# Optimization experiments

Measured on AMD Instinct MI355X. Metric: run time of the kernel, lower is better.

## Reference

```python
import jax, jax.numpy as jnp
import numpy as np
from jax import lax

B_, L_ = 4, 512
D_MODEL, N_LAYER = 384, 4
D_INNER, N_STATE, DT_RANK, D_CONV = 768, 16, 24, 4
VOCAB, FEAT = 1544, 1536


def setup_inputs() -> dict:
    key = jax.random.key(0)
    ks = iter(jax.random.split(key, 32))
    nrm = lambda shape, s=0.02: jax.random.normal(next(ks), shape, jnp.float32) * s
    input_ids = jax.random.normal(next(ks), (B_, L_, VOCAB), jnp.float32)
    return dict(
        input_ids=input_ids,
        fc_W=nrm((D_MODEL, VOCAB)), fc_b=jnp.zeros((D_MODEL,), jnp.float32),
        in_proj_W=nrm((N_LAYER, 2 * D_INNER, D_MODEL)),
        conv_W=nrm((N_LAYER, D_INNER, 1, D_CONV), 0.2),
        conv_b=jnp.zeros((N_LAYER, D_INNER), jnp.float32),
        x_proj_W=nrm((N_LAYER, DT_RANK + 2 * N_STATE, D_INNER)),
        dt_proj_W=nrm((N_LAYER, D_INNER, DT_RANK)),
        dt_proj_b=jnp.zeros((N_LAYER, D_INNER), jnp.float32),
        A_log=jnp.tile(jnp.log(jnp.arange(1, N_STATE + 1, dtype=jnp.float32)), (N_LAYER, D_INNER, 1)),
        D=jnp.ones((N_LAYER, D_INNER), jnp.float32),
        out_proj_W=nrm((N_LAYER, D_MODEL, D_INNER)),
        norm_W=jnp.ones((N_LAYER, D_MODEL), jnp.float32),
        normf_W=jnp.ones((D_MODEL,), jnp.float32),
        head_W=nrm((FEAT, D_MODEL)),
    )


def _rmsnorm(x, w, eps=1e-5):
    return x * lax.rsqrt(jnp.mean(x * x, axis=-1, keepdims=True) + eps) * w


def _selective_scan(u, delta, A, B, C, D):
    # u, delta: (b, l, d); A: (d, n); B, C: (b, l, n); D: (d,)
    dA = jnp.exp(jnp.einsum('bld,dn->bldn', delta, A))          # (b, l, d, n)
    dBu = jnp.einsum('bld,bln->bldn', delta * u, B)             # (b, l, d, n)
    b, l, d = u.shape
    n = A.shape[1]

    def step(h, inp):
        dA_t, dBu_t, c_t = inp                                   # (b,d,n),(b,d,n),(b,n)
        h = dA_t * h + dBu_t
        y = jnp.einsum('bdn,bn->bd', h, c_t)
        return h, y

    h0 = jnp.zeros((b, d, n), u.dtype)
    _, ys = lax.scan(step, h0, (dA.transpose(1, 0, 2, 3), dBu.transpose(1, 0, 2, 3), C.transpose(1, 0, 2)))
    return ys.transpose(1, 0, 2) + u * D                         # (b, l, d)


def _mamba(input_ids, fc_W, fc_b, in_proj_W, conv_W, conv_b, x_proj_W,
           dt_proj_W, dt_proj_b, A_log, D, out_proj_W, norm_W, normf_W, head_W):
    x = input_ids @ fc_W.T + fc_b                                # (b, l, d_model)
    for i in range(N_LAYER):
        h = _rmsnorm(x, norm_W[i])
        xz = h @ in_proj_W[i].T                                  # (b, l, 2*d_inner)
        xc, res = jnp.split(xz, 2, axis=-1)
        xc = xc.transpose(0, 2, 1)                               # (b, d_inner, l)
        xc = lax.conv_general_dilated(
            xc, conv_W[i], window_strides=(1,), padding=[(D_CONV - 1, 0)],
            feature_group_count=D_INNER, dimension_numbers=('NCH', 'OIH', 'NCH'))
        xc = xc + conv_b[i][None, :, None]
        u = jax.nn.silu(xc.transpose(0, 2, 1))                   # (b, l, d_inner)
        x_dbl = u @ x_proj_W[i].T
        delta, Bm, Cm = jnp.split(x_dbl, [DT_RANK, DT_RANK + N_STATE], axis=-1)
        delta = jax.nn.softplus(delta @ dt_proj_W[i].T + dt_proj_b[i])
        A = -jnp.exp(A_log[i])
        y = _selective_scan(u, delta, A, Bm, Cm, D[i])
        y = y * jax.nn.silu(res)
        x = y @ out_proj_W[i].T + x                              # residual
    x = _rmsnorm(x, normf_W)
    return x @ head_W.T                                          # (b, l, feat)


def reference(input_ids, fc_W, fc_b, in_proj_W, conv_W, conv_b, x_proj_W,
              dt_proj_W, dt_proj_b, A_log, D, out_proj_W, norm_W, normf_W, head_W):
    return _mamba(input_ids, fc_W, fc_b, in_proj_W, conv_W, conv_b, x_proj_W,
                  dt_proj_W, dt_proj_b, A_log, D, out_proj_W, norm_W, normf_W, head_W)
```

## Files before the change

### kernel.cpp

```cpp
#include <hip/hip_runtime.h>
#include <math.h>

#define B_ 4
#define L_ 512
#define MROWS 2048
#define D_MODEL 384
#define N_LAYER 4
#define D_INNER 768
#define N_STATE 16
#define DT_RANK 24
#define D_CONV 4
#define VOCAB 1544
#define FEAT 1536
#define XPROJ_N 56
#define NCH 16
#define SCH 32
#define DG 2

typedef __attribute__((ext_vector_type(8))) short short8;
typedef __attribute__((ext_vector_type(4))) float floatx4;

__device__ __forceinline__ float softplus_f(float x) { return x > 20.f ? x : log1pf(expf(x)); }
__device__ __forceinline__ float silu_f(float x) { return x / (1.f + __expf(-x)); }

__device__ __forceinline__ unsigned pack2bf(float x, float y) {
    unsigned ux = __float_as_uint(x); ux = (ux + 0x7FFFu + ((ux >> 16) & 1u)) >> 16;
    unsigned uy = __float_as_uint(y); uy = (uy + 0x7FFFu + ((uy >> 16) & 1u)) >> 16;
    return ux | (uy << 16);
}

template <int CTRL>
__device__ __forceinline__ float dpp_radd(float x) {
    int r = __builtin_amdgcn_update_dpp(0, __float_as_int(x), CTRL, 0xf, 0xf, true);
    return x + __int_as_float(r);
}

__device__ __forceinline__ void wave_lds_fence() {
    asm volatile("s_waitcnt lgkmcnt(0)" ::: "memory");
    __builtin_amdgcn_wave_barrier();
}

__device__ __forceinline__ short8 ld8h_guard(const short* __restrict__ p, int k, int ke) {
    if (k + 7 < ke) return *(const short8*)(p + k);
    short8 r = {0, 0, 0, 0, 0, 0, 0, 0};
#pragma unroll
    for (int j = 0; j < 8; ++j)
        if (k + j < ke) r[j] = p[k + j];
    return r;
}

struct CastDesc {
    const float* src[6];
    short*       dst[6];
    unsigned     cum[6];
};

__global__ __launch_bounds__(256) void cast_w_k(CastDesc cd, unsigned total4,
                                                float4* __restrict__ zb, unsigned z4)
{
    unsigned i = blockIdx.x * 256 + threadIdx.x;
    if (i < total4) {
        int s = 0;
#pragma unroll
        for (int j = 0; j < 5; ++j)
            if (i >= cd.cum[j] && s == j) s = j + 1;
        unsigned off = i - (s ? cd.cum[s - 1] : 0u);
        float4 v = ((const float4*)cd.src[s])[off];
        uint2 pk;
        pk.x = pack2bf(v.x, v.y);
        pk.y = pack2bf(v.z, v.w);
        ((uint2*)cd.dst[s])[off] = pk;
    } else {
        unsigned zi = i - total4;
        if (zi < z4) zb[zi] = make_float4(0.f, 0.f, 0.f, 0.f);
    }
}

__global__ __launch_bounds__(256) void rmsnorm_cast_k(
    const float* __restrict__ x, const float* __restrict__ nw,
    unsigned* __restrict__ outp)
{
    const int idx = blockIdx.x * 256 + threadIdx.x;
    const int row = idx >> 3, q = idx & 7;
    const float* xr = x + (size_t)row * D_MODEL + q * 48;
    float4 v[12];
    float s = 0.f;
#pragma unroll
    for (int i = 0; i < 12; ++i) {
        v[i] = *(const float4*)(xr + i * 4);
        s += v[i].x * v[i].x + v[i].y * v[i].y + v[i].z * v[i].z + v[i].w * v[i].w;
    }
    s += __shfl_xor(s, 1, 64);
    s += __shfl_xor(s, 2, 64);
    s += __shfl_xor(s, 4, 64);
    const float sc = rsqrtf(s / (float)D_MODEL + 1e-5f);
    unsigned* op = outp + ((size_t)row * D_MODEL + q * 48) / 2;
#pragma unroll
    for (int i = 0; i < 12; ++i) {
        float4 wv = *(const float4*)(nw + q * 48 + i * 4);
        op[i * 2]     = pack2bf(v[i].x * (sc * wv.x), v[i].y * (sc * wv.y));
        op[i * 2 + 1] = pack2bf(v[i].z * (sc * wv.z), v[i].w * (sc * wv.w));
    }
}

#define ASTR 40

template <int EPI, bool ATOMIC, bool NG, bool ABF>
__global__ __launch_bounds__(256) void mfma_gemm(
    const float* __restrict__ A, const short* __restrict__ Abf,
    const short* __restrict__ Wb,
    const float* __restrict__ bias,
    float* __restrict__ C, int M, int N, int K, int lda, int ldc, int KC)
{
    __shared__ short As[2][64 * ASTR];
    __shared__ short Ws[2][64 * ASTR];

    const int t  = threadIdx.x;
    const int m0 = blockIdx.y * 64;
    const int n0 = blockIdx.x * 64;
    const int ks = blockIdx.z * KC;
    const int ke = min(K, ks + KC);

    const int srow = t >> 2;
    const int sseg = (t & 3) * 8;

    short8 ra8, rw8;

    auto prefetch = [&](int k0) {
        ra8 = ld8h_guard(Abf + (size_t)(m0 + srow) * lda, k0 + sseg, ke);
        if (!NG || (n0 + srow) < N) {
            rw8 = ld8h_guard(Wb + (size_t)(n0 + srow) * (size_t)K, k0 + sseg, ke);
        } else {
            rw8 = (short8){0, 0, 0, 0, 0, 0, 0, 0};
        }
    };

    auto stage = [&](int p) {
        *(short8*)&As[p][srow * ASTR + sseg] = ra8;
        *(short8*)&Ws[p][srow * ASTR + sseg] = rw8;
    };

    prefetch(ks);
    stage(0);
    if (ks + 32 < ke) prefetch(ks + 32);
    __syncthreads();

    floatx4 acc[2][2];
#pragma unroll
    for (int i = 0; i < 2; ++i)
#pragma unroll
        for (int j = 0; j < 2; ++j) acc[i][j] = (floatx4){0.f, 0.f, 0.f, 0.f};

    const int w    = t >> 6;
    const int lane = t & 63;
    const int quad = lane >> 4;
    const int lm   = lane & 15;
    const int aoff = ((w >> 1) * 32 + lm) * ASTR + quad * 8;
    const int boff = ((w & 1) * 32 + lm) * ASTR + quad * 8;

    int p = 0;
    for (int k0 = ks; k0 < ke; k0 += 32) {
        const bool more = (k0 + 32 < ke);
        if (more) {
            stage(p ^ 1);
            if (k0 + 64 < ke) prefetch(k0 + 64);
        }
        short8 a0 = *(const short8*)&As[p][aoff];
        short8 a1 = *(const short8*)&As[p][aoff + 16 * ASTR];
        short8 b0 = *(const short8*)&Ws[p][boff];
        short8 b1 = *(const short8*)&Ws[p][boff + 16 * ASTR];
        acc[0][0] = __builtin_amdgcn_mfma_f32_16x16x32_bf16(a0, b0, acc[0][0], 0, 0, 0);
        acc[0][1] = __builtin_amdgcn_mfma_f32_16x16x32_bf16(a0, b1, acc[0][1], 0, 0, 0);
        acc[1][0] = __builtin_amdgcn_mfma_f32_16x16x32_bf16(a1, b0, acc[1][0], 0, 0, 0);
        acc[1][1] = __builtin_amdgcn_mfma_f32_16x16x32_bf16(a1, b1, acc[1][1], 0, 0, 0);
        if (more) {
            __syncthreads();
            p ^= 1;
        }
    }

    const int rbase = m0 + (w >> 1) * 32 + quad * 4;
    const int cbase = n0 + (w & 1) * 32 + lm;
#pragma unroll
    for (int mt = 0; mt < 2; ++mt)
#pragma unroll
        for (int nt = 0; nt < 2; ++nt) {
            const int gc = cbase + nt * 16;
            if (NG && gc >= N) continue;
#pragma unroll
            for (int r = 0; r < 4; ++r) {
                const size_t gr = rbase + mt * 16 + r;
                float v = acc[mt][nt][r];
                if (ATOMIC) {
                    if (EPI == 1 && blockIdx.z == 0) v += bias[gc];
                    atomicAdd(&C[gr * ldc + gc], v);
                } else {
                    if (EPI == 1) v += bias[gc];
                    if (EPI == 2) v = softplus_f(v + bias[gc]);
                    C[gr * ldc + gc] = v;
                }
            }
        }
}

__global__ __launch_bounds__(256) void conv_silu_k(
    const float* __restrict__ xz, const float* __restrict__ w,
    const float* __restrict__ cb, float* __restrict__ u, short* __restrict__ ubf)
{
    int idx = blockIdx.x * 256 + threadIdx.x;
    if (idx >= MROWS * (D_INNER / 4)) return;
    int dq = idx % (D_INNER / 4);
    int m  = idx / (D_INNER / 4);
    int d0 = dq * 4;
    int b = m / L_, l = m % L_;
    float4 wq[4];
#pragma unroll
    for (int j = 0; j < 4; ++j) wq[j] = *(const float4*)(w + (d0 + j) * D_CONV);
    float acc[4];
#pragma unroll
    for (int j = 0; j < 4; ++j) acc[j] = cb[d0 + j];
#pragma unroll
    for (int tt = 0; tt < 4; ++tt) {
        int ll = l - 3 + tt;
        if (ll >= 0) {
            float4 xv = *(const float4*)(xz + (size_t)(b * L_ + ll) * (2 * D_INNER) + d0);
            acc[0] = fmaf(xv.x, ((const float*)&wq[0])[tt], acc[0]);
            acc[1] = fmaf(xv.y, ((const float*)&wq[1])[tt], acc[1]);
            acc[2] = fmaf(xv.z, ((const float*)&wq[2])[tt], acc[2]);
            acc[3] = fmaf(xv.w, ((const float*)&wq[3])[tt], acc[3]);
        }
    }
    float4 o = make_float4(silu_f(acc[0]), silu_f(acc[1]), silu_f(acc[2]), silu_f(acc[3]));
    *(float4*)(u + (size_t)m * D_INNER + d0) = o;
    uint2 pk;
    pk.x = pack2bf(o.x, o.y);
    pk.y = pack2bf(o.z, o.w);
    *(uint2*)(ubf + (size_t)m * D_INNER + d0) = pk;
}

__global__ __launch_bounds__(512, 4) void scan_fused_k(
    const float* __restrict__ xdbl, const float* __restrict__ u,
    const float* __restrict__ xz,
    const float* __restrict__ dtW, const float* __restrict__ dtb,
    const float* __restrict__ A_log, const float* __restrict__ Dp,
    short* __restrict__ ybf)
{
    __shared__ __align__(16) float2 sdu[NCH][SCH][DG];
    __shared__ __align__(16) float  sy[NCH][SCH][DG];
    __shared__ __align__(16) float2 sPH[NCH][DG][16];

    const int t  = threadIdx.x;
    const int w  = t >> 6;
    const int l  = t & 63;
    const int ch = l >> 5;
    const int c  = w * 2 + ch;
    const int dl = (l >> 4) & 1;
    const int n  = l & 15;
    const int bx  = blockIdx.x;
    const int dgi = (bx & 7) * (D_INNER / DG / 8) + (bx >> 3);
    const int d0 = dgi * DG;
    const int d  = d0 + dl;
    const int b  = blockIdx.y;

    const int tc = t >> 5, tj = t & 31;
    const size_t trow = (size_t)b * L_ + t;

    float2 rv  = *(const float2*)(xz + trow * (2 * D_INNER) + D_INNER + d0);
    float2 uv2 = *(const float2*)(u + trow * D_INNER + d0);
    float2 Dv  = *(const float2*)(Dp + d0);

    {
        const float* wd = dtW + (size_t)d0 * DT_RANK;
        const float* xr = xdbl + trow * XPROJ_N;
        float acc0 = dtb[d0];
        float acc1 = dtb[d0 + 1];
#pragma unroll
        for (int q = 0; q < 6; ++q) {
            float4 xv = *(const float4*)(xr + q * 4);
            float4 w0 = *(const float4*)(wd + q * 4);
            float4 w1 = *(const float4*)(wd + DT_RANK + q * 4);
            acc0 = fmaf(xv.x, w0.x, acc0); acc0 = fmaf(xv.y, w0.y, acc0);
            acc0 = fmaf(xv.z, w0.z, acc0); acc0 = fmaf(xv.w, w0.w, acc0);
            acc1 = fmaf(xv.x, w1.x, acc1); acc1 = fmaf(xv.y, w1.y, acc1);
            acc1 = fmaf(xv.z, w1.z, acc1); acc1 = fmaf(xv.w, w1.w, acc1);
        }
        float4 pk = make_float4(softplus_f(acc0), uv2.x, softplus_f(acc1), uv2.y);
        *(float4*)&sdu[tc][tj][0] = pk;
    }
    wave_lds_fence();

    const float Av = -expf(A_log[d * N_STATE + n]);
    const float* xbn = xdbl + ((size_t)b * L_ + c * SCH) * XPROJ_N + DT_RANK + n;

    float eA[SCH], cc[SCH];
    {
        float h = 0.f, sdv = 0.f;
        float rB[8];
#pragma unroll
        for (int q = 0; q < 8; ++q) rB[q] = xbn[q * XPROJ_N];
#pragma unroll
        for (int g = 0; g < SCH / 8; ++g) {
            float nB[8];
            if (g + 1 < SCH / 8) {
#pragma unroll
                for (int q = 0; q < 8; ++q) nB[q] = xbn[(g * 8 + 8 + q) * XPROJ_N];
            }
#pragma unroll
            for (int q = 0; q < 8; ++q) {
                const int j = g * 8 + q;
                float2 du = *(const float2*)&sdu[c][j][dl];
                float e  = __expf(du.x * Av);
                float tt = du.x * du.y * rB[q];
                eA[j] = e;
                cc[j] = tt;
                h = fmaf(e, h, tt);
                sdv += du.x;
            }
#pragma unroll
            for (int q = 0; q < 8; ++q) rB[q] = nB[q];
        }
        float2 ph;
        ph.x = __expf(sdv * Av);
        ph.y = h;
        *(float2*)&sPH[c][dl][n] = ph;
    }

    float rC[8];
#pragma unroll
    for (int q = 0; q < 8; ++q) rC[q] = xbn[q * XPROJ_N + N_STATE];
    __syncthreads();

    float hs = 0.f;
#pragma unroll
    for (int s = 0; s < NCH - 1; ++s) {
        float2 ph = *(const float2*)&sPH[s][dl][n];
        const bool m = s < c;
        hs = fmaf(m ? ph.x : 1.f, hs, m ? ph.y : 0.f);
    }

    {
        float h = hs;
#pragma unroll
        for (int g = 0; g < SCH / 8; ++g) {
            float nC[8];
            if (g + 1 < SCH / 8) {
#pragma unroll
                for (int q = 0; q < 8; ++q)
                    nC[q] = xbn[(g * 8 + 8 + q) * XPROJ_N + N_STATE];
            }
#pragma unroll
            for (int q = 0; q < 8; ++q) {
                const int j = g * 8 + q;
                h = fmaf(eA[j], h, cc[j]);
                float p = h * rC[q];
                p = dpp_radd<0x128>(p);
                p = dpp_radd<0x124>(p);
                p = dpp_radd<0x122>(p);
                p = dpp_radd<0x121>(p);
                if (n == 0) sy[c][j][dl] = p;
            }
#pragma unroll
            for (int q = 0; q < 8; ++q) rC[q] = nC[q];
        }
    }
    wave_lds_fence();

    {
        float2 yv = *(const float2*)&sy[tc][tj][0];
        float y0 = fmaf(uv2.x, Dv.x, yv.x);
        float y1 = fmaf(uv2.y, Dv.y, yv.y);
        float o0 = y0 * silu_f(rv.x);
        float o1 = y1 * silu_f(rv.y);
        *(unsigned*)(ybf + trow * D_INNER + d0) = pack2bf(o0, o1);
    }
}

extern "C" void kernel_launch(void* const* d_in, const int* in_sizes, int n_in,
                              void* d_out, int out_size, void* d_ws, size_t ws_size,
                              hipStream_t stream)
{
    const float* input_ids = (const float*)d_in[0];
    const float* fc_W      = (const float*)d_in[1];
    const float* fc_b      = (const float*)d_in[2];
    const float* in_proj_W = (const float*)d_in[3];
    const float* conv_W    = (const float*)d_in[4];
    const float* conv_b    = (const float*)d_in[5];
    const float* x_proj_W  = (const float*)d_in[6];
    const float* dt_proj_W = (const float*)d_in[7];
    const float* dt_proj_b = (const float*)d_in[8];
    const float* A_log     = (const float*)d_in[9];
    const float* Dp        = (const float*)d_in[10];
    const float* out_proj_W= (const float*)d_in[11];
    const float* norm_W    = (const float*)d_in[12];
    const float* normf_W   = (const float*)d_in[13];
    const float* head_W    = (const float*)d_in[14];
    float* out = (float*)d_out;

    float* ws       = (float*)d_ws;
    float* x_ws     = ws;
    float* xdbl_ws  = x_ws    + (size_t)MROWS * D_MODEL;
    float* xz_ws    = xdbl_ws + (size_t)N_LAYER * MROWS * XPROJ_N;
    float* u_ws     = xz_ws   + (size_t)MROWS * 2 * D_INNER;
    short* bf       = (short*)(u_ws + (size_t)MROWS * D_INNER);
    short* wbf_fc   = bf;
    short* wbf_in   = wbf_fc  + (size_t)D_MODEL * VOCAB;
    short* wbf_x    = wbf_in  + (size_t)N_LAYER * 2 * D_INNER * D_MODEL;
    short* wbf_out  = wbf_x   + (size_t)N_LAYER * XPROJ_N * D_INNER;
    short* wbf_head = wbf_out + (size_t)N_LAYER * D_MODEL * D_INNER;
    short* ids_bf   = wbf_head+ (size_t)FEAT * D_MODEL;
    short* ubf_ws   = ids_bf  + (size_t)MROWS * VOCAB;
    short* ybf_ws   = ubf_ws  + (size_t)MROWS * D_INNER;
    short* xnorm_bf = ybf_ws  + (size_t)MROWS * D_INNER;

    const dim3 blk(256);
    const dim3 blk512(512);

    CastDesc cd;
    cd.src[0] = fc_W;       cd.dst[0] = wbf_fc;
    cd.src[1] = in_proj_W;  cd.dst[1] = wbf_in;
    cd.src[2] = x_proj_W;   cd.dst[2] = wbf_x;
    cd.src[3] = out_proj_W; cd.dst[3] = wbf_out;
    cd.src[4] = head_W;     cd.dst[4] = wbf_head;
    cd.src[5] = input_ids;  cd.dst[5] = ids_bf;
    unsigned c0 = (unsigned)(D_MODEL * VOCAB / 4);
    unsigned c1 = c0 + (unsigned)(N_LAYER * 2 * D_INNER * D_MODEL / 4);
    unsigned c2 = c1 + (unsigned)(N_LAYER * XPROJ_N * D_INNER / 4);
    unsigned c3 = c2 + (unsigned)(N_LAYER * D_MODEL * D_INNER / 4);
    unsigned c4 = c3 + (unsigned)(FEAT * D_MODEL / 4);
    unsigned c5 = c4 + (unsigned)(MROWS * VOCAB / 4);
    cd.cum[0] = c0; cd.cum[1] = c1; cd.cum[2] = c2;
    cd.cum[3] = c3; cd.cum[4] = c4; cd.cum[5] = c5;
    const unsigned zero4 = (unsigned)((MROWS * D_MODEL + N_LAYER * MROWS * XPROJ_N) / 4);
    cast_w_k<<<(c5 + zero4 + 255) / 256, blk, 0, stream>>>(cd, c5, (float4*)x_ws, zero4);

    mfma_gemm<1, true, false, true><<<dim3(D_MODEL / 64, MROWS / 64, 7), blk, 0, stream>>>(
        nullptr, ids_bf, wbf_fc, fc_b, x_ws,
        MROWS, D_MODEL, VOCAB, VOCAB, D_MODEL, 256);

    for (int i = 0; i < N_LAYER; ++i) {
        float* xdbl_i = xdbl_ws + (size_t)i * MROWS * XPROJ_N;

        rmsnorm_cast_k<<<MROWS * 8 / 256, blk, 0, stream>>>(
            x_ws, norm_W + i * D_MODEL, (unsigned*)xnorm_bf);

        mfma_gemm<0, false, false, true><<<dim3(2 * D_INNER / 64, MROWS / 64, 1), blk, 0, stream>>>(
            nullptr, xnorm_bf, wbf_in + (size_t)i * 2 * D_INNER * D_MODEL,
            nullptr, xz_ws,
            MROWS, 2 * D_INNER, D_MODEL, D_MODEL, 2 * D_INNER, D_MODEL);

        conv_silu_k<<<(MROWS * (D_INNER / 4) + 255) / 256, blk, 0, stream>>>(
            xz_ws, conv_W + (size_t)i * D_INNER * D_CONV, conv_b + i * D_INNER,
            u_ws, ubf_ws);

        mfma_gemm<0, true, true, true><<<dim3(1, MROWS / 64, 6), blk, 0, stream>>>(
            nullptr, ubf_ws, wbf_x + (size_t)i * XPROJ_N * D_INNER,
            nullptr, xdbl_i,
            MROWS, XPROJ_N, D_INNER, D_INNER, XPROJ_N, 128);

        scan_fused_k<<<dim3(D_INNER / DG, B_), blk512, 0, stream>>>(
            xdbl_i, u_ws, xz_ws,
            dt_proj_W + (size_t)i * D_INNER * DT_RANK, dt_proj_b + i * D_INNER,
            A_log + (size_t)i * D_INNER * N_STATE, Dp + i * D_INNER, ybf_ws);

        mfma_gemm<0, true, false, true><<<dim3(D_MODEL / 64, MROWS / 64, 2), blk, 0, stream>>>(
            nullptr, ybf_ws, wbf_out + (size_t)i * D_MODEL * D_INNER,
            nullptr, x_ws,
            MROWS, D_MODEL, D_INNER, D_INNER, D_MODEL, 384);
    }

    rmsnorm_cast_k<<<MROWS * 8 / 256, blk, 0, stream>>>(
        x_ws, normf_W, (unsigned*)xnorm_bf);
    mfma_gemm<0, false, false, true><<<dim3(FEAT / 64, MROWS / 64, 1), blk, 0, stream>>>(
        nullptr, xnorm_bf, wbf_head, nullptr, out,
        MROWS, FEAT, D_MODEL, D_MODEL, FEAT, D_MODEL);
}
```

Baseline: 437.8 us.

## Fuse depthwise conv+SiLU into the x_proj MFMA GEMM prologue

Replaces the separate conv_silu kernel and the x_proj GEMM with one kernel. It loads a 67-row xz slab into shared memory, computes the causal depthwise conv and SiLU, writes u in fp32, and feeds bf16 u straight into the MFMA tiles, with split-K atomics into xdbl. This drops one launch per layer plus the bf16 u buffer's write and read. In exchange the K loop is serialized with extra syncs, and each block redoes a small overlap of conv work for its halo rows. The unused fp32-A template parameter is also removed from the GEMM.

```diff
diff --git a/kernel.cpp b/kernel.cpp
--- a/kernel.cpp
+++ b/kernel.cpp
@@ -105,9 +105,9 @@
 
 #define ASTR 40
 
-template <int EPI, bool ATOMIC, bool NG, bool ABF>
+template <int EPI, bool ATOMIC, bool NG>
 __global__ __launch_bounds__(256) void mfma_gemm(
-    const float* __restrict__ A, const short* __restrict__ Abf,
+    const short* __restrict__ Abf,
     const short* __restrict__ Wb,
     const float* __restrict__ bias,
     float* __restrict__ C, int M, int N, int K, int lda, int ldc, int KC)
@@ -203,39 +203,127 @@
         }
 }
 
-__global__ __launch_bounds__(256) void conv_silu_k(
-    const float* __restrict__ xz, const float* __restrict__ w,
-    const float* __restrict__ cb, float* __restrict__ u, short* __restrict__ ubf)
+__global__ __launch_bounds__(256) void xproj_conv_k(
+    const float* __restrict__ xz, const short* __restrict__ Wb,
+    const float* __restrict__ cw, const float* __restrict__ cbp,
+    float* __restrict__ u, float* __restrict__ xdbl)
 {
-    int idx = blockIdx.x * 256 + threadIdx.x;
-    if (idx >= MROWS * (D_INNER / 4)) return;
-    int dq = idx % (D_INNER / 4);
-    int m  = idx / (D_INNER / 4);
-    int d0 = dq * 4;
-    int b = m / L_, l = m % L_;
-    float4 wq[4];
-#pragma unroll
-    for (int j = 0; j < 4; ++j) wq[j] = *(const float4*)(w + (d0 + j) * D_CONV);
-    float acc[4];
-#pragma unroll
-    for (int j = 0; j < 4; ++j) acc[j] = cb[d0 + j];
-#pragma unroll
-    for (int tt = 0; tt < 4; ++tt) {
-        int ll = l - 3 + tt;
-        if (ll >= 0) {
-            float4 xv = *(const float4*)(xz + (size_t)(b * L_ + ll) * (2 * D_INNER) + d0);
-            acc[0] = fmaf(xv.x, ((const float*)&wq[0])[tt], acc[0]);
-            acc[1] = fmaf(xv.y, ((const float*)&wq[1])[tt], acc[1]);
-            acc[2] = fmaf(xv.z, ((const float*)&wq[2])[tt], acc[2]);
-            acc[3] = fmaf(xv.w, ((const float*)&wq[3])[tt], acc[3]);
-        }
-    }
-    float4 o = make_float4(silu_f(acc[0]), silu_f(acc[1]), silu_f(acc[2]), silu_f(acc[3]));
-    *(float4*)(u + (size_t)m * D_INNER + d0) = o;
-    uint2 pk;
-    pk.x = pack2bf(o.x, o.y);
-    pk.y = pack2bf(o.z, o.w);
-    *(uint2*)(ubf + (size_t)m * D_INNER + d0) = pk;
+    __shared__ float xs[67][33];
+    __shared__ short As[64 * ASTR];
+    __shared__ short Ws[64 * ASTR];
+
+    const int t  = threadIdx.x;
+    const int m0 = blockIdx.x * 64;
+    const int z  = blockIdx.y;
+    const int l0 = m0 & 511;
+
+    const int srow = t >> 2;
+    const int sseg = (t & 3) * 8;
+
+    float4 slab[3];
+    auto load_slab = [&](int kc) {
+#pragma unroll
+        for (int q = 0; q < 3; ++q) {
+            const int idx = t + q * 256;
+            if (idx < 536) {
+                const int r = idx >> 3, s = idx & 7;
+                const int g = m0 - 3 + r;
+                slab[q] = (g >= 0)
+                    ? *(const float4*)(xz + (size_t)g * (2 * D_INNER) + kc + s * 4)
+                    : make_float4(0.f, 0.f, 0.f, 0.f);
+            }
+        }
+    };
+    short8 rw8;
+    auto load_w = [&](int kc) {
+        if (srow < XPROJ_N) rw8 = *(const short8*)(Wb + (size_t)srow * D_INNER + kc + sseg);
+        else rw8 = (short8){0, 0, 0, 0, 0, 0, 0, 0};
+    };
+
+    floatx4 acc[2][2];
+#pragma unroll
+    for (int i = 0; i < 2; ++i)
+#pragma unroll
+        for (int j = 0; j < 2; ++j) acc[i][j] = (floatx4){0.f, 0.f, 0.f, 0.f};
+
+    const int w    = t >> 6;
+    const int lane = t & 63;
+    const int quad = lane >> 4;
+    const int lm   = lane & 15;
+    const int aoff = ((w >> 1) * 32 + lm) * ASTR + quad * 8;
+    const int boff = ((w & 1) * 32 + lm) * ASTR + quad * 8;
+
+    load_slab(z * 128);
+    load_w(z * 128);
+
+    for (int step = 0; step < 4; ++step) {
+        const int kc = z * 128 + step * 32;
+#pragma unroll
+        for (int q = 0; q < 3; ++q) {
+            const int idx = t + q * 256;
+            if (idx < 536) {
+                const int r = idx >> 3, s = idx & 7;
+                *(float4*)&xs[r][s * 4] = slab[q];
+            }
+        }
+        __syncthreads();
+
+        {
+            const int l = l0 + srow;
+            float a[8];
+#pragma unroll
+            for (int j = 0; j < 8; ++j) a[j] = cbp[kc + sseg + j];
+#pragma unroll
+            for (int j = 0; j < 8; ++j) {
+                const int ch = sseg + j;
+                const float4 wj = *(const float4*)(cw + (size_t)(kc + ch) * 4);
+#pragma unroll
+                for (int tt = 0; tt < 4; ++tt) {
+                    if (l - 3 + tt >= 0)
+                        a[j] = fmaf(xs[srow + tt][ch], ((const float*)&wj)[tt], a[j]);
+                }
+            }
+            float o[8];
+#pragma unroll
+            for (int j = 0; j < 8; ++j) o[j] = silu_f(a[j]);
+            float* up = u + (size_t)(m0 + srow) * D_INNER + kc + sseg;
+            *(float4*)up       = make_float4(o[0], o[1], o[2], o[3]);
+            *(float4*)(up + 4) = make_float4(o[4], o[5], o[6], o[7]);
+            int4 pa;
+            pa.x = pack2bf(o[0], o[1]); pa.y = pack2bf(o[2], o[3]);
+            pa.z = pack2bf(o[4], o[5]); pa.w = pack2bf(o[6], o[7]);
+            *(int4*)&As[srow * ASTR + sseg] = pa;
+            *(short8*)&Ws[srow * ASTR + sseg] = rw8;
+        }
+        __syncthreads();
+
+        if (step + 1 < 4) { load_slab(kc + 32); load_w(kc + 32); }
+
+        short8 a0 = *(const short8*)&As[aoff];
+        short8 a1 = *(const short8*)&As[aoff + 16 * ASTR];
+        short8 b0 = *(const short8*)&Ws[boff];
+        short8 b1 = *(const short8*)&Ws[boff + 16 * ASTR];
+        acc[0][0] = __builtin_amdgcn_mfma_f32_16x16x32_bf16(a0, b0, acc[0][0], 0, 0, 0);
+        acc[0][1] = __builtin_amdgcn_mfma_f32_16x16x32_bf16(a0, b1, acc[0][1], 0, 0, 0);
+        acc[1][0] = __builtin_amdgcn_mfma_f32_16x16x32_bf16(a1, b0, acc[1][0], 0, 0, 0);
+        acc[1][1] = __builtin_amdgcn_mfma_f32_16x16x32_bf16(a1, b1, acc[1][1], 0, 0, 0);
+        if (step + 1 < 4) __syncthreads();
+    }
+
+    const int rbase = m0 + (w >> 1) * 32 + quad * 4;
+    const int cbase = (w & 1) * 32 + lm;
+#pragma unroll
+    for (int mt = 0; mt < 2; ++mt)
+#pragma unroll
+        for (int nt = 0; nt < 2; ++nt) {
+            const int gc = cbase + nt * 16;
+            if (gc >= XPROJ_N) continue;
+#pragma unroll
+            for (int r = 0; r < 4; ++r) {
+                const size_t gr = rbase + mt * 16 + r;
+                atomicAdd(&xdbl[gr * XPROJ_N + gc], acc[mt][nt][r]);
+            }
+        }
 }
 
 __global__ __launch_bounds__(512, 4) void scan_fused_k(
@@ -408,8 +496,7 @@
     short* wbf_out  = wbf_x   + (size_t)N_LAYER * XPROJ_N * D_INNER;
     short* wbf_head = wbf_out + (size_t)N_LAYER * D_MODEL * D_INNER;
     short* ids_bf   = wbf_head+ (size_t)FEAT * D_MODEL;
-    short* ubf_ws   = ids_bf  + (size_t)MROWS * VOCAB;
-    short* ybf_ws   = ubf_ws  + (size_t)MROWS * D_INNER;
+    short* ybf_ws   = ids_bf  + (size_t)MROWS * VOCAB;
     short* xnorm_bf = ybf_ws  + (size_t)MROWS * D_INNER;
 
     const dim3 blk(256);
@@ -433,8 +520,8 @@
     const unsigned zero4 = (unsigned)((MROWS * D_MODEL + N_LAYER * MROWS * XPROJ_N) / 4);
     cast_w_k<<<(c5 + zero4 + 255) / 256, blk, 0, stream>>>(cd, c5, (float4*)x_ws, zero4);
 
-    mfma_gemm<1, true, false, true><<<dim3(D_MODEL / 64, MROWS / 64, 7), blk, 0, stream>>>(
-        nullptr, ids_bf, wbf_fc, fc_b, x_ws,
+    mfma_gemm<1, true, false><<<dim3(D_MODEL / 64, MROWS / 64, 7), blk, 0, stream>>>(
+        ids_bf, wbf_fc, fc_b, x_ws,
         MROWS, D_MODEL, VOCAB, VOCAB, D_MODEL, 256);
 
     for (int i = 0; i < N_LAYER; ++i) {
@@ -443,34 +530,30 @@
         rmsnorm_cast_k<<<MROWS * 8 / 256, blk, 0, stream>>>(
             x_ws, norm_W + i * D_MODEL, (unsigned*)xnorm_bf);
 
-        mfma_gemm<0, false, false, true><<<dim3(2 * D_INNER / 64, MROWS / 64, 1), blk, 0, stream>>>(
-            nullptr, xnorm_bf, wbf_in + (size_t)i * 2 * D_INNER * D_MODEL,
+        mfma_gemm<0, false, false><<<dim3(2 * D_INNER / 64, MROWS / 64, 1), blk, 0, stream>>>(
+            xnorm_bf, wbf_in + (size_t)i * 2 * D_INNER * D_MODEL,
             nullptr, xz_ws,
             MROWS, 2 * D_INNER, D_MODEL, D_MODEL, 2 * D_INNER, D_MODEL);
 
-        conv_silu_k<<<(MROWS * (D_INNER / 4) + 255) / 256, blk, 0, stream>>>(
-            xz_ws, conv_W + (size_t)i * D_INNER * D_CONV, conv_b + i * D_INNER,
-            u_ws, ubf_ws);
-
-        mfma_gemm<0, true, true, true><<<dim3(1, MROWS / 64, 6), blk, 0, stream>>>(
-            nullptr, ubf_ws, wbf_x + (size_t)i * XPROJ_N * D_INNER,
-            nullptr, xdbl_i,
-            MROWS, XPROJ_N, D_INNER, D_INNER, XPROJ_N, 128);
+        xproj_conv_k<<<dim3(MROWS / 64, 6), blk, 0, stream>>>(
+            xz_ws, wbf_x + (size_t)i * XPROJ_N * D_INNER,
+            conv_W + (size_t)i * D_INNER * D_CONV, conv_b + i * D_INNER,
+            u_ws, xdbl_i);
 
         scan_fused_k<<<dim3(D_INNER / DG, B_), blk512, 0, stream>>>(
             xdbl_i, u_ws, xz_ws,
             dt_proj_W + (size_t)i * D_INNER * DT_RANK, dt_proj_b + i * D_INNER,
             A_log + (size_t)i * D_INNER * N_STATE, Dp + i * D_INNER, ybf_ws);
 
-        mfma_gemm<0, true, false, true><<<dim3(D_MODEL / 64, MROWS / 64, 2), blk, 0, stream>>>(
-            nullptr, ybf_ws, wbf_out + (size_t)i * D_MODEL * D_INNER,
+        mfma_gemm<0, true, false><<<dim3(D_MODEL / 64, MROWS / 64, 2), blk, 0, stream>>>(
+            ybf_ws, wbf_out + (size_t)i * D_MODEL * D_INNER,
             nullptr, x_ws,
             MROWS, D_MODEL, D_INNER, D_INNER, D_MODEL, 384);
     }
 
     rmsnorm_cast_k<<<MROWS * 8 / 256, blk, 0, stream>>>(
         x_ws, normf_W, (unsigned*)xnorm_bf);
-    mfma_gemm<0, false, false, true><<<dim3(FEAT / 64, MROWS / 64, 1), blk, 0, stream>>>(
-        nullptr, xnorm_bf, wbf_head, nullptr, out,
+    mfma_gemm<0, false, false><<<dim3(FEAT / 64, MROWS / 64, 1), blk, 0, stream>>>(
+        xnorm_bf, wbf_head, nullptr, out,
         MROWS, FEAT, D_MODEL, D_MODEL, FEAT, D_MODEL);
 }
```

After: 447.8 us. +2.3%, slower.
